# Performance work log

Measured on AMD Instinct MI355X. Metric: run time of the kernel, lower is better.

## Reference

```python
import jax, jax.numpy as jnp
import numpy as np

B, H, W, DIM, NH = 4, 32, 32, 768, 12
HD = DIM // NH  # head_dim = 64


def setup_inputs() -> dict:
    key = jax.random.key(0)
    ks = jax.random.split(key, 12)
    n = lambda i, shape, s=1.0: jax.random.normal(ks[i], shape, jnp.float32) * s
    return {
        "q": n(0, (B, H, W, DIM)),
        "k": n(1, (B, H, W, DIM)),
        "v": n(2, (B, H, W, DIM)),
        # Linear weights stored as (in, out) so y = x @ W + b (equivalent to torch x @ W.T)
        "Wq": n(3, (DIM, DIM), 0.02), "bq": jnp.zeros((DIM,), jnp.float32),
        "Wk": n(4, (DIM, DIM), 0.02), "bk": jnp.zeros((DIM,), jnp.float32),
        "Wv": n(5, (DIM, DIM), 0.02), "bv": jnp.zeros((DIM,), jnp.float32),
        "Wp": n(6, (DIM, DIM), 0.02), "bp": jnp.zeros((DIM,), jnp.float32),
        # decomposed relative position tables: (2*size - 1, head_dim)
        "rel_pos_h": n(7, (2 * H - 1, HD), 0.02),
        "rel_pos_w": n(8, (2 * W - 1, HD), 0.02),
    }


def reference(q, k, v, Wq, bq, Wk, bk, Wv, bv, Wp, bp, rel_pos_h, rel_pos_w):
    scale = HD ** -0.5

    def to_heads(x, Wt, b):
        y = x.reshape(B, H * W, DIM) @ Wt + b          # (B, HW, DIM)
        return y.reshape(B, H * W, NH, HD).transpose(0, 2, 1, 3).reshape(B * NH, H * W, HD)

    qh = to_heads(q, Wq, bq)   # (B*NH, HW, HD)
    kh = to_heads(k, Wk, bk)
    vh = to_heads(v, Wv, bv)

    # scaled dot-product scores
    attn = jnp.einsum('bqd,bkd->bqk', qh * scale, kh)  # (B*NH, HW, HW)

    # decomposed relative position bias (q_size == k_size == input_size, no interpolation)
    idx_h = jnp.arange(H)[:, None] - jnp.arange(H)[None, :] + (H - 1)
    idx_w = jnp.arange(W)[:, None] - jnp.arange(W)[None, :] + (W - 1)
    Rh = rel_pos_h[idx_h]  # (H, H, HD)
    Rw = rel_pos_w[idx_w]  # (W, W, HD)
    rq = qh.reshape(B * NH, H, W, HD)  # unscaled q, as in torch add_decomposed_rel_pos
    rel_h = jnp.einsum('bhwc,hkc->bhwk', rq, Rh)  # (B*NH, H, W, H)
    rel_w = jnp.einsum('bhwc,wkc->bhwk', rq, Rw)  # (B*NH, H, W, W)

    attn = (attn.reshape(B * NH, H, W, H, W)
            + rel_h[:, :, :, :, None]
            + rel_w[:, :, :, None, :]).reshape(B * NH, H * W, H * W)

    attn = jax.nn.softmax(attn, axis=-1)
    x = (attn @ vh).reshape(B, NH, H, W, HD).transpose(0, 2, 3, 1, 4).reshape(B, H, W, DIM)
    return x @ Wp + bp
```

## Files before the change

kernel.cpp:

```cpp
#include <hip/hip_runtime.h>
#include <math.h>

#define DIM  768
#define NH   12
#define HD   64
#define HWN  1024
#define MROWS 4096

typedef __attribute__((ext_vector_type(8))) short short8;
typedef __attribute__((ext_vector_type(4))) float f32x4;
typedef _Float16 h8 __attribute__((ext_vector_type(8)));
typedef _Float16 h2 __attribute__((ext_vector_type(2)));

__device__ __forceinline__ void gl_lds16(const void* g, void* l) {
    __builtin_amdgcn_global_load_lds(
        (const __attribute__((address_space(1))) void*)g,
        (__attribute__((address_space(3))) void*)l, 16, 0, 0);
}

__global__ __launch_bounds__(256) void wconv_kernel(
    const float* __restrict__ Wq, const float* __restrict__ Wk,
    const float* __restrict__ Wv, const float* __restrict__ Wp,
    _Float16* __restrict__ WtAll)
{
    __shared__ float Ws[64][65];
    const int z = blockIdx.z;
    const float* W = (z == 0) ? Wq : (z == 1) ? Wk : (z == 2) ? Wv : Wp;
    _Float16* Wt = WtAll + (size_t)z * 589824;

    const int k0 = blockIdx.y * 64, n0 = blockIdx.x * 64;
    const int t = threadIdx.x;
    {
        int r = t >> 2, c4 = (t & 3) * 16;
        #pragma unroll
        for (int u = 0; u < 16; u += 4)
            *(float4*)&Ws[r][c4 + u] = *(const float4*)(W + (size_t)(k0 + r) * DIM + n0 + c4 + u);
    }
    __syncthreads();
    const int n = t >> 2, kseg = (t & 3) * 16;
    h8 h0, h1;
    #pragma unroll
    for (int j = 0; j < 8; ++j) {
        h0[j] = (_Float16)Ws[kseg + j][n];
        h1[j] = (_Float16)Ws[kseg + 8 + j][n];
    }
    size_t base = (size_t)(n0 + n) * DIM + k0 + kseg;
    *(h8*)(Wt + base) = h0;
    *(h8*)(Wt + base + 8) = h1;
}

__global__ __launch_bounds__(256) void rel2frag_kernel(
    const float* __restrict__ rph, const float* __restrict__ rpw,
    _Float16* __restrict__ relTg)
{
    const int t = threadIdx.x;
    const int row = t >> 1, c0 = (t & 1) * 32;
    const float* src = (row < 63) ? rph + (size_t)row * HD
                     : (row >= 64 && row < 127) ? rpw + (size_t)(row - 64) * HD
                     : nullptr;
    #pragma unroll
    for (int g = 0; g < 4; ++g) {
        h8 o;
        #pragma unroll
        for (int j = 0; j < 8; ++j)
            o[j] = src ? (_Float16)src[c0 + g * 8 + j] : (_Float16)0.0f;
        *(h8*)(relTg + (size_t)row * HD + c0 + g * 8) = o;
    }
}

template<int AMODE>
__global__ __launch_bounds__(256, 3) void gemm_mfma_kernel(
    const void* __restrict__ X0, const void* __restrict__ X1,
    const void* __restrict__ X2, const _Float16* __restrict__ WtAll,
    const float* __restrict__ bias0, const float* __restrict__ bias1,
    const float* __restrict__ bias2,
    void* __restrict__ Y0, void* __restrict__ Y1, void* __restrict__ Y2)
{
    __shared__ __align__(16) char smem[AMODE == 0 ? 40960 : 24576];
    const int BOFF = (AMODE == 0) ? 32768 : 16384;
    const int t = threadIdx.x;
    const int w = t >> 6, lane = t & 63;
    const int l15 = lane & 15, l4 = lane >> 4;

    int sel, rem;
    if (AMODE == 0) {
        const int sw = (blockIdx.x & 7) * 144 + (blockIdx.x >> 3);
        sel = sw / 384; rem = sw - sel * 384;
    } else {
        const int sw = (blockIdx.x & 7) * 48 + (blockIdx.x >> 3);
        sel = 3; rem = sw;
    }
    const int rb = rem / 12, cb = rem - rb * 12;
    const int row0 = rb * 128, col0 = cb * 64;

    const char* Ab = (const char*)((AMODE == 1 || sel == 0) ? X0 : (sel == 1) ? X1 : X2);
    const _Float16* Bt = WtAll + (size_t)sel * 589824;
    const float* bias = (AMODE == 1) ? bias0 : (sel == 0) ? bias0 : (sel == 1) ? bias1 : bias2;

    f32x4 acc[4][2];
    #pragma unroll
    for (int i = 0; i < 4; ++i)
        #pragma unroll
        for (int j = 0; j < 2; ++j) acc[i][j] = (f32x4){0, 0, 0, 0};

    for (int kt = 0; kt < 12; ++kt) {
        if (AMODE == 0) {
            #pragma unroll
            for (int i = 0; i < 8; ++i) {
                const int fi = w * 8 + i;
                const int row = fi * 4 + (lane >> 4);
                const int real = ((lane & 15) * 16) ^ ((row & 7) << 5);
                gl_lds16(Ab + (size_t)(row0 + row) * 3072 + kt * 256 + real, smem + fi * 1024);
            }
        } else {
            #pragma unroll
            for (int i = 0; i < 4; ++i) {
                const int fi = w * 4 + i;
                const int row = fi * 8 + (lane >> 3);
                const int real = ((lane & 7) * 16) ^ ((row & 7) << 4);
                gl_lds16(Ab + (size_t)(row0 + row) * 1536 + kt * 128 + real, smem + fi * 1024);
            }
        }
        #pragma unroll
        for (int it = 0; it < 2; ++it) {
            const int f = it * 4 + w;
            const int ks = f >> 2, cf = f & 3;
            const size_t off = (size_t)(col0 + cf * 16 + l15) * 1536 + kt * 128 + ks * 64 + l4 * 16;
            gl_lds16((const char*)Bt + off, smem + BOFF + f * 1024);
        }
        __syncthreads();

        __builtin_amdgcn_s_setprio(1);
        #pragma unroll
        for (int ks = 0; ks < 2; ++ks) {
            const int fb = ks * 4 + (w & 1) * 2;
            h8 b0 = *(const h8*)(smem + BOFF + (fb    ) * 1024 + lane * 16);
            h8 b1 = *(const h8*)(smem + BOFF + (fb + 1) * 1024 + lane * 16);
            #pragma unroll
            for (int rf = 0; rf < 4; ++rf) {
                const int arow = (w >> 1) * 64 + rf * 16 + l15;
                h8 ah;
                if (AMODE == 0) {
                    const int base = arow * 256 + ((ks * 128 + l4 * 32) ^ ((arow & 7) << 5));
                    f32x4 a0 = *(const f32x4*)(smem + base);
                    f32x4 a1 = *(const f32x4*)(smem + base + 16);
                    ah[0] = (_Float16)a0[0]; ah[1] = (_Float16)a0[1];
                    ah[2] = (_Float16)a0[2]; ah[3] = (_Float16)a0[3];
                    ah[4] = (_Float16)a1[0]; ah[5] = (_Float16)a1[1];
                    ah[6] = (_Float16)a1[2]; ah[7] = (_Float16)a1[3];
                } else {
                    const int base = arow * 128 + ((ks * 64 + l4 * 16) ^ ((arow & 7) << 4));
                    ah = *(const h8*)(smem + base);
                }
                acc[rf][0] = __builtin_amdgcn_mfma_f32_16x16x32_f16(ah, b0, acc[rf][0], 0, 0, 0);
                acc[rf][1] = __builtin_amdgcn_mfma_f32_16x16x32_f16(ah, b1, acc[rf][1], 0, 0, 0);
            }
        }
        __builtin_amdgcn_s_setprio(0);
        __syncthreads();
    }

    const int wrow0 = row0 + (w >> 1) * 64;
    const int wcol0 = col0 + (w & 1) * 32;
    #pragma unroll
    for (int cf = 0; cf < 2; ++cf) {
        const int c = wcol0 + cf * 16 + l15;
        const float bb = bias[c];
        #pragma unroll
        for (int rf = 0; rf < 4; ++rf) {
            #pragma unroll
            for (int reg = 0; reg < 4; ++reg) {
                const int r = wrow0 + rf * 16 + l4 * 4 + reg;
                float y = acc[rf][cf][reg] + bb;
                if (AMODE == 1) {
                    ((float*)Y0)[(size_t)r * DIM + c] = y;
                } else {
                    _Float16* Yh = (_Float16*)((sel == 0) ? Y0 : (sel == 1) ? Y1 : Y2);
                    size_t base = ((size_t)((r >> 10) * NH + cb) * HWN + (r & 1023)) * HD + (c - col0);
                    Yh[base] = (_Float16)y;
                }
            }
        }
    }
}

#define AT_REL   0
#define AT_VT    8704
#define AT_P     25088
#define AT_KB    33280
#define AT_QF    8704
#define AT_RELT  17920
#define AT_PG    17920
#define AT_OF    8704
#define AT_TOTAL 49664

__global__ __launch_bounds__(256, 3) void attn_kernel(
    const _Float16* __restrict__ qh, const _Float16* __restrict__ kh,
    const _Float16* __restrict__ vh, const _Float16* __restrict__ relTg,
    _Float16* __restrict__ aout)
{
    __shared__ __align__(16) char smem[AT_TOTAL];
    const int bid = blockIdx.x;
    const int j   = bid >> 3;
    const int bh  = (bid & 7) * 6 + (j >> 4);
    const int qb  = j & 15;
    const int t  = threadIdx.x;
    const int w  = t >> 6;
    const int lane = t & 63;
    const int l15 = lane & 15, l4 = lane >> 4;

    _Float16* Rel = (_Float16*)(smem + AT_REL);
    _Float16* Qf  = (_Float16*)(smem + AT_QF);

    const int r = t >> 2, dc = (t & 3) * 16;
    {
        const _Float16* qp = qh + ((size_t)bh * HWN + qb * 64 + r) * HD + dc;
        *(short8*)(&Qf[r * 72 + dc])     = *(const short8*)(qp);
        *(short8*)(&Qf[r * 72 + dc + 8]) = *(const short8*)(qp + 8);
        #pragma unroll
        for (int it = 0; it < 4; ++it) {
            const int f = it * 4 + w;
            const int ct = f >> 1, ks = f & 1;
            gl_lds16((const char*)relTg + (ct * 16 + l15) * 128 + ks * 64 + l4 * 16,
                     smem + AT_RELT + f * 1024);
        }
    }
    __syncthreads();

    const _Float16* kb_ = kh + (size_t)bh * HWN * HD;
    const _Float16* vb_ = vh + (size_t)bh * HWN * HD;
    const int key2 = (t & 31) * 2, dgrp = t >> 5;
    short8 rv0, rv1;
#define LOADV(KT) {                                                            \
        const _Float16* vp = vb_ + (size_t)((KT) * 64 + key2) * HD + dgrp * 8; \
        rv0 = *(const short8*)vp; rv1 = *(const short8*)(vp + HD); }
    LOADV(0);

    h8 qf2[2];
    {
        const int qr = w * 16 + l15;
        qf2[0] = *(const h8*)(&Qf[qr * 72 + l4 * 8]);
        qf2[1] = *(const h8*)(&Qf[qr * 72 + 32 + l4 * 8]);
        #pragma unroll
        for (int j2 = 0; j2 < 8; ++j2) { qf2[0][j2] *= (_Float16)0.125f; qf2[1][j2] *= (_Float16)0.125f; }
    }

    f32x4 pacc[4][2];
    #pragma unroll
    for (int i = 0; i < 4; ++i)
        #pragma unroll
        for (int j2 = 0; j2 < 2; ++j2) pacc[i][j2] = (f32x4){0, 0, 0, 0};
    #pragma unroll
    for (int ks = 0; ks < 2; ++ks) {
        h8 b0 = *(const h8*)(smem + AT_RELT + ((w * 2 + 0) * 2 + ks) * 1024 + lane * 16);
        h8 b1 = *(const h8*)(smem + AT_RELT + ((w * 2 + 1) * 2 + ks) * 1024 + lane * 16);
        #pragma unroll
        for (int rt = 0; rt < 4; ++rt) {
            h8 a = *(const h8*)(&Qf[(rt * 16 + l15) * 72 + ks * 32 + l4 * 8]);
            pacc[rt][0] = __builtin_amdgcn_mfma_f32_16x16x32_f16(a, b0, pacc[rt][0], 0, 0, 0);
            pacc[rt][1] = __builtin_amdgcn_mfma_f32_16x16x32_f16(a, b1, pacc[rt][1], 0, 0, 0);
        }
    }

    __syncthreads();
    _Float16* Pg = (_Float16*)(smem + AT_PG);
    #pragma unroll
    for (int rt = 0; rt < 4; ++rt)
        #pragma unroll
        for (int cb2 = 0; cb2 < 2; ++cb2)
            #pragma unroll
            for (int reg = 0; reg < 4; ++reg)
                Pg[(rt * 16 + l4 * 4 + reg) * 130 + w * 32 + cb2 * 16 + l15] =
                    (_Float16)pacc[rt][cb2][reg];
    __syncthreads();

    {
        const int q = t >> 2, kk0 = (t & 3) * 8;
        const int hw = qb * 64 + q;
        const int hq = hw >> 5, wq = hw & 31;
        short8 vh_, vw_;
        #pragma unroll
        for (int j2 = 0; j2 < 8; ++j2) {
            const int kk = kk0 + j2;
            vh_[j2] = *(const short*)&Pg[q * 130 + (hq + 31 - kk)];
            vw_[j2] = *(const short*)&Pg[q * 130 + 64 + (wq + 31 - kk)];
        }
        *(short8*)(&Rel[q * 68 + kk0])      = vh_;
        *(short8*)(&Rel[q * 68 + 32 + kk0]) = vw_;
    }
    __syncthreads();

    const int qrow_bias = w * 16 + l15;
    float rw_[2][4];
    #pragma unroll
    for (int c2 = 0; c2 < 2; ++c2)
        #pragma unroll
        for (int reg = 0; reg < 4; ++reg)
            rw_[c2][reg] = (float)Rel[qrow_bias * 68 + 32 + c2 * 16 + l4 * 4 + reg];

#define STAGEK(KT, BUF) {                                                      \
        _Pragma("unroll")                                                      \
        for (int i2 = 0; i2 < 2; ++i2) {                                       \
            const int f = w * 2 + i2;                                          \
            const int keyk = f * 8 + (lane >> 3);                              \
            const int srcb = ((lane & 7) * 16) ^ ((lane >> 3) << 4);           \
            gl_lds16((const char*)kb_ + (size_t)((KT) * 64 + keyk) * 128 + srcb, \
                     smem + AT_KB + (BUF) * 8192 + f * 1024);                  \
        } }

#define WRITEVT(BUF) {                                                         \
        _Pragma("unroll")                                                      \
        for (int j2 = 0; j2 < 8; ++j2) {                                       \
            const int d = dgrp * 8 + j2;                                       \
            unsigned pk = ((unsigned short)rv0[j2]) |                          \
                          (((unsigned)(unsigned short)rv1[j2]) << 16);         \
            *(unsigned*)(smem + AT_VT + (BUF) * 8192 + d * 128 +               \
                         ((key2 * 2) ^ ((d & 7) << 4))) = pk; } }
    WRITEVT(0);
    STAGEK(0, 0);

    f32x4 acc_o[4] = {{0,0,0,0},{0,0,0,0},{0,0,0,0},{0,0,0,0}};
    float m_ = -INFINITY, l_ = 0.f;
    char* Pw = smem + AT_P + w * 2048;
    const int swzP = (l15 & 7) << 4;

    #pragma unroll 2
    for (int kt = 0; kt < 16; ++kt) {
        const int cur = kt & 1;
        __syncthreads();
        if (kt < 15) { LOADV(kt + 1); STAGEK(kt + 1, cur ^ 1); }

        const float rh0 = (float)Rel[qrow_bias * 68 + kt * 2];
        const float rh1 = (float)Rel[qrow_bias * 68 + kt * 2 + 1];
        f32x4 accs[4];
        #pragma unroll
        for (int ct = 0; ct < 4; ++ct) {
            const float rhc = (ct >> 1) ? rh1 : rh0;
            #pragma unroll
            for (int reg = 0; reg < 4; ++reg)
                accs[ct][reg] = rw_[ct & 1][reg] + rhc;
        }
        __builtin_amdgcn_s_setprio(1);
        #pragma unroll
        for (int ct = 0; ct < 4; ++ct) {
            const int row = ct * 16 + l15;
            const int swzK = (row & 7) << 4;
            #pragma unroll
            for (int ks = 0; ks < 2; ++ks) {
                h8 kfr = *(const h8*)(smem + AT_KB + cur * 8192 + row * 128 +
                                      ((ks * 64 + l4 * 16) ^ swzK));
                accs[ct] = __builtin_amdgcn_mfma_f32_16x16x32_f16(kfr, qf2[ks], accs[ct], 0, 0, 0);
            }
        }
        __builtin_amdgcn_s_setprio(0);

        float mx[4];
        #pragma unroll
        for (int ct = 0; ct < 4; ++ct)
            mx[ct] = fmaxf(fmaxf(accs[ct][0], accs[ct][1]),
                           fmaxf(accs[ct][2], accs[ct][3]));
        float tmax = fmaxf(fmaxf(mx[0], mx[1]), fmaxf(mx[2], mx[3]));
        tmax = fmaxf(tmax, __shfl_xor(tmax, 16));
        tmax = fmaxf(tmax, __shfl_xor(tmax, 32));

        if (__any(tmax > m_ + 8.f)) {
            const float mnew = fmaxf(m_, tmax);
            const float factor = __expf(m_ - mnew);
            m_ = mnew;
            l_ *= factor;
            #pragma unroll
            for (int reg = 0; reg < 4; ++reg) {
                const float fr = __shfl(factor, l4 * 4 + reg);
                #pragma unroll
                for (int dt = 0; dt < 4; ++dt) acc_o[dt][reg] *= fr;
            }
        }

        float tsum = 0.f;
        #pragma unroll
        for (int ct = 0; ct < 4; ++ct) {
            float p0 = __expf(accs[ct][0] - m_);
            float p1 = __expf(accs[ct][1] - m_);
            float p2 = __expf(accs[ct][2] - m_);
            float p3 = __expf(accs[ct][3] - m_);
            tsum += (p0 + p1) + (p2 + p3);
            h2 pa = {(_Float16)p0, (_Float16)p1};
            h2 pb = {(_Float16)p2, (_Float16)p3};
            uint2 pk;
            pk.x = *(unsigned*)&pa;
            pk.y = *(unsigned*)&pb;
            *(uint2*)(Pw + l15 * 128 + ((ct * 32 + l4 * 8) ^ swzP)) = pk;
        }
        tsum += __shfl_xor(tsum, 16);
        tsum += __shfl_xor(tsum, 32);
        l_ += tsum;

        __builtin_amdgcn_s_setprio(1);
        #pragma unroll
        for (int ks = 0; ks < 2; ++ks) {
            h8 pa = *(const h8*)(Pw + l15 * 128 + ((ks * 64 + l4 * 16) ^ swzP));
            #pragma unroll
            for (int dt = 0; dt < 4; ++dt) {
                const int d = dt * 16 + l15;
                h8 vf = *(const h8*)(smem + AT_VT + cur * 8192 + d * 128 +
                                     ((ks * 64 + l4 * 16) ^ ((d & 7) << 4)));
                acc_o[dt] = __builtin_amdgcn_mfma_f32_16x16x32_f16(pa, vf, acc_o[dt], 0, 0, 0);
            }
        }
        __builtin_amdgcn_s_setprio(0);

        if (kt < 15) WRITEVT(cur ^ 1);
    }

    const float invl = 1.0f / l_;
    float linv[4];
    #pragma unroll
    for (int reg = 0; reg < 4; ++reg) linv[reg] = __shfl(invl, l4 * 4 + reg);
    __syncthreads();
    _Float16* Of = (_Float16*)(smem + AT_OF);
    #pragma unroll
    for (int reg = 0; reg < 4; ++reg) {
        const int qloc = w * 16 + l4 * 4 + reg;
        #pragma unroll
        for (int dt = 0; dt < 4; ++dt)
            Of[qloc * 72 + dt * 16 + l15] = (_Float16)(acc_o[dt][reg] * linv[reg]);
    }
    __syncthreads();
    {
        const int b_ = bh / NH, nh = bh % NH;
        _Float16* op = aout + ((size_t)b_ * HWN + qb * 64 + r) * DIM + nh * HD + dc;
        *(short8*)op       = *(const short8*)(&Of[r * 72 + dc]);
        *(short8*)(op + 8) = *(const short8*)(&Of[r * 72 + dc + 8]);
    }
}

extern "C" void kernel_launch(void* const* d_in, const int* in_sizes, int n_in,
                              void* d_out, int out_size, void* d_ws, size_t ws_size,
                              hipStream_t stream) {
    const float* q   = (const float*)d_in[0];
    const float* k   = (const float*)d_in[1];
    const float* v   = (const float*)d_in[2];
    const float* Wq  = (const float*)d_in[3];
    const float* bq  = (const float*)d_in[4];
    const float* Wk  = (const float*)d_in[5];
    const float* bk  = (const float*)d_in[6];
    const float* Wv  = (const float*)d_in[7];
    const float* bv  = (const float*)d_in[8];
    const float* Wp  = (const float*)d_in[9];
    const float* bp  = (const float*)d_in[10];
    const float* rph = (const float*)d_in[11];
    const float* rpw = (const float*)d_in[12];

    float* out = (float*)d_out;
    char*  w0  = (char*)d_ws;

    _Float16* wtAll = (_Float16*)(w0);
    _Float16* relTg = (_Float16*)(w0 + 4718592);
    _Float16* qf16  = (_Float16*)(w0 + 4734976);
    _Float16* kf16  = (_Float16*)(w0 + 11026432);
    _Float16* vf16  = (_Float16*)(w0 + 17317888);
    _Float16* aout  = (_Float16*)(w0 + 23609344);

    dim3 blk(256);
    wconv_kernel<<<dim3(12, 12, 4), blk, 0, stream>>>(Wq, Wk, Wv, Wp, wtAll);
    rel2frag_kernel<<<1, blk, 0, stream>>>(rph, rpw, relTg);
    gemm_mfma_kernel<0><<<1152, blk, 0, stream>>>(
        q, k, v, wtAll, bq, bk, bv, qf16, kf16, vf16);
    attn_kernel<<<768, blk, 0, stream>>>(qf16, kf16, vf16, relTg, aout);
    gemm_mfma_kernel<1><<<384, blk, 0, stream>>>(
        aout, nullptr, nullptr, wtAll, bp, nullptr, nullptr,
        out, nullptr, nullptr);
}
```

Before: 101.5 us.

## Pre-convert QKV inputs to fp16 and widen QKV GEMM tile to 128 columns

Adds a separate kernel that converts q, k and v from fp32 to fp16 once, so the QKV projection GEMM loads fp16 A tiles instead of converting fp32 in LDS. With the A data halved, the QKV GEMM tile grows to 128x128 (576 blocks instead of 1152), which improves reuse of A per block. Each block now writes across two heads, so the output indexing is derived from the column. This adds an extra launch and a full read and write of the fp16 copies, and the workspace is reshuffled so the attention output buffer aliases the fp16 input buffer.

```diff
diff --git a/kernel.cpp b/kernel.cpp
--- a/kernel.cpp
+++ b/kernel.cpp
@@ -16,6 +16,24 @@
     __builtin_amdgcn_global_load_lds(
         (const __attribute__((address_space(1))) void*)g,
         (__attribute__((address_space(3))) void*)l, 16, 0, 0);
+}
+
+__global__ __launch_bounds__(256) void xconv_kernel(
+    const float* __restrict__ q, const float* __restrict__ k,
+    const float* __restrict__ v, _Float16* __restrict__ xf16)
+{
+    const int N8 = MROWS * DIM / 8;
+    int i = blockIdx.x * 256 + threadIdx.x;
+    const int stride = gridDim.x * 256;
+    for (; i < 3 * N8; i += stride) {
+        const int sel = i / N8, j = i - sel * N8;
+        const float* src = (sel == 0) ? q : (sel == 1) ? k : v;
+        float4 a0 = ((const float4*)src)[j * 2];
+        float4 a1 = ((const float4*)src)[j * 2 + 1];
+        h8 o = {(_Float16)a0.x, (_Float16)a0.y, (_Float16)a0.z, (_Float16)a0.w,
+                (_Float16)a1.x, (_Float16)a1.y, (_Float16)a1.z, (_Float16)a1.w};
+        *(h8*)(xf16 + (size_t)sel * (MROWS * DIM) + (size_t)j * 8) = o;
+    }
 }
 
 __global__ __launch_bounds__(256) void wconv_kernel(
@@ -70,61 +88,55 @@
 
 template<int AMODE>
 __global__ __launch_bounds__(256, 3) void gemm_mfma_kernel(
-    const void* __restrict__ X0, const void* __restrict__ X1,
-    const void* __restrict__ X2, const _Float16* __restrict__ WtAll,
+    const _Float16* __restrict__ X0, const _Float16* __restrict__ WtAll,
     const float* __restrict__ bias0, const float* __restrict__ bias1,
     const float* __restrict__ bias2,
     void* __restrict__ Y0, void* __restrict__ Y1, void* __restrict__ Y2)
 {
-    __shared__ __align__(16) char smem[AMODE == 0 ? 40960 : 24576];
-    const int BOFF = (AMODE == 0) ? 32768 : 16384;
+    constexpr int NT  = (AMODE == 0) ? 128 : 64;
+    constexpr int NBF = NT / 16;
+    constexpr int WCF = NT / 32;
+    __shared__ __align__(16) char smem[16384 + 2 * NBF * 1024];
+    constexpr int BOFF = 16384;
+
     const int t = threadIdx.x;
     const int w = t >> 6, lane = t & 63;
     const int l15 = lane & 15, l4 = lane >> 4;
 
-    int sel, rem;
+    int sel, rem, rb, cb;
     if (AMODE == 0) {
-        const int sw = (blockIdx.x & 7) * 144 + (blockIdx.x >> 3);
-        sel = sw / 384; rem = sw - sel * 384;
+        const int sw = (blockIdx.x & 7) * 72 + (blockIdx.x >> 3);
+        sel = sw / 192; rem = sw - sel * 192;
+        rb = rem / 6; cb = rem - rb * 6;
     } else {
         const int sw = (blockIdx.x & 7) * 48 + (blockIdx.x >> 3);
         sel = 3; rem = sw;
-    }
-    const int rb = rem / 12, cb = rem - rb * 12;
-    const int row0 = rb * 128, col0 = cb * 64;
-
-    const char* Ab = (const char*)((AMODE == 1 || sel == 0) ? X0 : (sel == 1) ? X1 : X2);
+        rb = rem / 12; cb = rem - rb * 12;
+    }
+    const int row0 = rb * 128, col0 = cb * NT;
+
+    const char* Ab = (const char*)(X0 + (AMODE == 0 ? (size_t)sel * (MROWS * DIM) : 0));
     const _Float16* Bt = WtAll + (size_t)sel * 589824;
     const float* bias = (AMODE == 1) ? bias0 : (sel == 0) ? bias0 : (sel == 1) ? bias1 : bias2;
 
-    f32x4 acc[4][2];
+    f32x4 acc[4][WCF];
     #pragma unroll
     for (int i = 0; i < 4; ++i)
         #pragma unroll
-        for (int j = 0; j < 2; ++j) acc[i][j] = (f32x4){0, 0, 0, 0};
+        for (int j = 0; j < WCF; ++j) acc[i][j] = (f32x4){0, 0, 0, 0};
 
     for (int kt = 0; kt < 12; ++kt) {
-        if (AMODE == 0) {
-            #pragma unroll
-            for (int i = 0; i < 8; ++i) {
-                const int fi = w * 8 + i;
-                const int row = fi * 4 + (lane >> 4);
-                const int real = ((lane & 15) * 16) ^ ((row & 7) << 5);
-                gl_lds16(Ab + (size_t)(row0 + row) * 3072 + kt * 256 + real, smem + fi * 1024);
-            }
-        } else {
-            #pragma unroll
-            for (int i = 0; i < 4; ++i) {
-                const int fi = w * 4 + i;
-                const int row = fi * 8 + (lane >> 3);
-                const int real = ((lane & 7) * 16) ^ ((row & 7) << 4);
-                gl_lds16(Ab + (size_t)(row0 + row) * 1536 + kt * 128 + real, smem + fi * 1024);
-            }
-        }
-        #pragma unroll
-        for (int it = 0; it < 2; ++it) {
+        #pragma unroll
+        for (int i = 0; i < 4; ++i) {
+            const int fi = w * 4 + i;
+            const int row = fi * 8 + (lane >> 3);
+            const int srcb = ((lane & 7) * 16) ^ ((row & 7) << 4);
+            gl_lds16(Ab + (size_t)(row0 + row) * 1536 + kt * 128 + srcb, smem + fi * 1024);
+        }
+        #pragma unroll
+        for (int it = 0; it < 2 * NBF / 4; ++it) {
             const int f = it * 4 + w;
-            const int ks = f >> 2, cf = f & 3;
+            const int ks = f / NBF, cf = f % NBF;
             const size_t off = (size_t)(col0 + cf * 16 + l15) * 1536 + kt * 128 + ks * 64 + l4 * 16;
             gl_lds16((const char*)Bt + off, smem + BOFF + f * 1024);
         }
@@ -133,27 +145,20 @@
         __builtin_amdgcn_s_setprio(1);
         #pragma unroll
         for (int ks = 0; ks < 2; ++ks) {
-            const int fb = ks * 4 + (w & 1) * 2;
-            h8 b0 = *(const h8*)(smem + BOFF + (fb    ) * 1024 + lane * 16);
-            h8 b1 = *(const h8*)(smem + BOFF + (fb + 1) * 1024 + lane * 16);
+            h8 b[WCF];
+            #pragma unroll
+            for (int cf4 = 0; cf4 < WCF; ++cf4) {
+                const int fb = ks * NBF + (w & 1) * WCF + cf4;
+                b[cf4] = *(const h8*)(smem + BOFF + fb * 1024 + lane * 16);
+            }
             #pragma unroll
             for (int rf = 0; rf < 4; ++rf) {
                 const int arow = (w >> 1) * 64 + rf * 16 + l15;
-                h8 ah;
-                if (AMODE == 0) {
-                    const int base = arow * 256 + ((ks * 128 + l4 * 32) ^ ((arow & 7) << 5));
-                    f32x4 a0 = *(const f32x4*)(smem + base);
-                    f32x4 a1 = *(const f32x4*)(smem + base + 16);
-                    ah[0] = (_Float16)a0[0]; ah[1] = (_Float16)a0[1];
-                    ah[2] = (_Float16)a0[2]; ah[3] = (_Float16)a0[3];
-                    ah[4] = (_Float16)a1[0]; ah[5] = (_Float16)a1[1];
-                    ah[6] = (_Float16)a1[2]; ah[7] = (_Float16)a1[3];
-                } else {
-                    const int base = arow * 128 + ((ks * 64 + l4 * 16) ^ ((arow & 7) << 4));
-                    ah = *(const h8*)(smem + base);
-                }
-                acc[rf][0] = __builtin_amdgcn_mfma_f32_16x16x32_f16(ah, b0, acc[rf][0], 0, 0, 0);
-                acc[rf][1] = __builtin_amdgcn_mfma_f32_16x16x32_f16(ah, b1, acc[rf][1], 0, 0, 0);
+                const int base = arow * 128 + ((ks * 64 + l4 * 16) ^ ((arow & 7) << 4));
+                h8 ah = *(const h8*)(smem + base);
+                #pragma unroll
+                for (int cf4 = 0; cf4 < WCF; ++cf4)
+                    acc[rf][cf4] = __builtin_amdgcn_mfma_f32_16x16x32_f16(ah, b[cf4], acc[rf][cf4], 0, 0, 0);
             }
         }
         __builtin_amdgcn_s_setprio(0);
@@ -161,22 +166,22 @@
     }
 
     const int wrow0 = row0 + (w >> 1) * 64;
-    const int wcol0 = col0 + (w & 1) * 32;
-    #pragma unroll
-    for (int cf = 0; cf < 2; ++cf) {
-        const int c = wcol0 + cf * 16 + l15;
-        const float bb = bias[c];
+    const int wcol0 = col0 + (w & 1) * (WCF * 16);
+    #pragma unroll
+    for (int cf4 = 0; cf4 < WCF; ++cf4) {
+        const int c = wcol0 + cf4 * 16 + l15;
+        const float bb = bias[c - (AMODE == 0 ? 0 : col0) + (AMODE == 0 ? 0 : col0)];
         #pragma unroll
         for (int rf = 0; rf < 4; ++rf) {
             #pragma unroll
             for (int reg = 0; reg < 4; ++reg) {
                 const int r = wrow0 + rf * 16 + l4 * 4 + reg;
-                float y = acc[rf][cf][reg] + bb;
+                float y = acc[rf][cf4][reg] + bb;
                 if (AMODE == 1) {
                     ((float*)Y0)[(size_t)r * DIM + c] = y;
                 } else {
                     _Float16* Yh = (_Float16*)((sel == 0) ? Y0 : (sel == 1) ? Y1 : Y2);
-                    size_t base = ((size_t)((r >> 10) * NH + cb) * HWN + (r & 1023)) * HD + (c - col0);
+                    size_t base = ((size_t)((r >> 10) * NH + (c >> 6)) * HWN + (r & 1023)) * HD + (c & 63);
                     Yh[base] = (_Float16)y;
                 }
             }
@@ -456,18 +461,19 @@
 
     _Float16* wtAll = (_Float16*)(w0);
     _Float16* relTg = (_Float16*)(w0 + 4718592);
-    _Float16* qf16  = (_Float16*)(w0 + 4734976);
-    _Float16* kf16  = (_Float16*)(w0 + 11026432);
-    _Float16* vf16  = (_Float16*)(w0 + 17317888);
-    _Float16* aout  = (_Float16*)(w0 + 23609344);
+    _Float16* xf16  = (_Float16*)(w0 + 4734976);
+    _Float16* aout  = (_Float16*)(w0 + 4734976);
+    _Float16* qf16  = (_Float16*)(w0 + 23609344);
+    _Float16* kf16  = (_Float16*)(w0 + 29900800);
+    _Float16* vf16  = (_Float16*)(w0 + 36192256);
 
     dim3 blk(256);
+    xconv_kernel<<<2048, blk, 0, stream>>>(q, k, v, xf16);
     wconv_kernel<<<dim3(12, 12, 4), blk, 0, stream>>>(Wq, Wk, Wv, Wp, wtAll);
     rel2frag_kernel<<<1, blk, 0, stream>>>(rph, rpw, relTg);
-    gemm_mfma_kernel<0><<<1152, blk, 0, stream>>>(
-        q, k, v, wtAll, bq, bk, bv, qf16, kf16, vf16);
+    gemm_mfma_kernel<0><<<576, blk, 0, stream>>>(
+        xf16, wtAll, bq, bk, bv, qf16, kf16, vf16);
     attn_kernel<<<768, blk, 0, stream>>>(qf16, kf16, vf16, relTg, aout);
     gemm_mfma_kernel<1><<<384, blk, 0, stream>>>(
-        aout, nullptr, nullptr, wtAll, bp, nullptr, nullptr,
-        out, nullptr, nullptr);
-}
+        aout, wtAll, bp, nullptr, nullptr, out, nullptr, nullptr);
+}
```

Result: no change. 100.3 us (-1.2%).
